# Kernel tuning notes

Measured on AMD Instinct MI355X. Metric: run time of the kernel, lower is better.

Reference implementation:

```python
import jax, jax.numpy as jnp
import numpy as np

B = 2_000_000   # time steps (the module's 'batch' axis is the sequential time axis)
SEQ = 1
IN = 2
SPIN = 365
TRAIN = 1_000_000


def setup_inputs() -> dict:
    key = jax.random.key(0)
    ks = jax.random.split(key, 9)
    x = jax.random.uniform(ks[0], (B, SEQ, IN), dtype=jnp.float32)
    y_obs = jax.random.uniform(ks[1], (B, 1), dtype=jnp.float32)
    c_mean = jax.random.uniform(ks[2], (1,), dtype=jnp.float32)
    c_std = jax.random.uniform(ks[3], (1,), dtype=jnp.float32) + 0.5  # keep away from 0
    weight_r_yom = jax.random.uniform(ks[4], (1, 1), dtype=jnp.float32)
    weight_r_ylm = jax.random.uniform(ks[5], (1, 1), dtype=jnp.float32)
    weight_r_yfm = jax.random.uniform(ks[6], (1, 1), dtype=jnp.float32)
    bias_b0_yom = jax.random.uniform(ks[7], (1,), dtype=jnp.float32)
    weight_b1_yom = jax.random.uniform(ks[8], (1, 1), dtype=jnp.float32)
    return dict(x=x, epoch=1, time_lag=0, y_obs=y_obs, c_mean=c_mean, c_std=c_std,
                weight_r_yom=weight_r_yom, weight_r_ylm=weight_r_ylm,
                weight_r_yfm=weight_r_yfm, bias_b0_yom=bias_b0_yom,
                weight_b1_yom=weight_b1_yom)


def _forward(x, y_obs, c_mean, c_std, weight_r_yom, weight_r_ylm, weight_r_yfm,
             bias_b0_yom, weight_b1_yom, time_lag):
    # hidden_size == 1 -> scalar cell state. Original loop order: b outer, t inner,
    # i.e. steps visit x[b, t] in row-major order; per-b outputs keep the last t value.
    Bn, S, _ = x.shape
    steps = x.reshape(Bn * S, 2)[time_lag * S:]            # rows b < time_lag are skipped
    wo, wl, wf = weight_r_yom[0, 0], weight_r_ylm[0, 0], weight_r_yfm[0, 0]
    b0, wb1 = bias_b0_yom[0], weight_b1_yom[0, 0]
    mo, so = c_mean[0], c_std[0]
    eo, el, ef = jnp.exp(wo), jnp.exp(wl), jnp.exp(wf)
    denom = eo + el + ef
    oo1 = eo / denom                                        # softmax-like gate weights
    ol1 = el / denom
    obsstd = jnp.std(y_obs[SPIN:TRAIN], ddof=1)             # torch.std is unbiased (ddof=1)

    def step(c, u):
        u1, u2 = u[0], u[1]
        oo = oo1 * jax.nn.sigmoid(b0 + (c - mo) / so * wb1)  # output gate
        safe_c = jnp.where(c > 0, c, jnp.float32(1.0))
        olc = jnp.where(c > 0, ol1 - jax.nn.relu(ol1 - u2 / safe_c), ol1)  # PET-clamped leak
        f = 1.0 - oo - olc                                   # mass-conserving forget gate
        c_next = f * c + u1
        # per-step stored values use the PRE-update state c (c_0 in original)
        return c_next, (oo * c, c, ol1 * c, olc * c, oo, olc, f)

    _, (q, cs, ls, lcs, goo, golc, gf) = jax.lax.scan(step, jnp.float32(0.0), steps)

    def per_b(v):
        v = v.reshape(-1, S)[:, -1]          # keep last inner-t value per b
        v = jnp.pad(v, (time_lag, 0))        # skipped rows stay zero
        return v[:, None]                    # [B, 1]

    h_n = per_b(q)                           # bp_0 == 0, so h_n == q_n == oo * c_0
    c_n = per_b(cs)
    l_n = per_b(ls)
    lc_n = per_b(lcs)
    Gate_oo = per_b(goo)
    Gate_olc = per_b(golc)
    Gate_f = per_b(gf)
    processed = (jnp.arange(Bn)[:, None] >= time_lag)
    Gate_ol = jnp.where(processed, ol1, 0.0).astype(x.dtype)
    obs_std = jnp.where(processed, obsstd, 0.0).astype(x.dtype)
    zeros = jnp.zeros((Bn, 1), x.dtype)      # bp_n and Gate_ib (ib == 0 always)
    h_nout = jnp.concatenate([h_n, obs_std], axis=1)
    return (h_n, c_n, l_n, lc_n, zeros, zeros, Gate_oo, Gate_ol, Gate_olc, Gate_f,
            h_nout, obs_std)


def reference(x, epoch, time_lag, y_obs, c_mean, c_std, weight_r_yom, weight_r_ylm,
              weight_r_yfm, bias_b0_yom, weight_b1_yom):
    return _forward(x, y_obs, c_mean, c_std, weight_r_yom, weight_r_ylm,
                    weight_r_yfm, bias_b0_yom, weight_b1_yom, int(time_lag))
```

## Files before the change

### kernel.cpp

```cpp
#include <hip/hip_runtime.h>
#include <math.h>

#define SPIN 365
#define TRAIN 1000000
#define WARM 64
#define L 8
#define BLK 512
#define RPB (L * BLK)
#define NSTAGE (RPB + WARM)
#define NPART 256


__global__ void partial_std_kernel(const float* __restrict__ y, double* __restrict__ part) {
    int tid = blockIdx.x * blockDim.x + threadIdx.x;
    int stride = gridDim.x * blockDim.x;
    double s = 0.0, s2 = 0.0;
    for (int i = SPIN + tid; i < TRAIN; i += stride) {
        double v = (double)y[i];
        s += v;
        s2 += v * v;
    }
    for (int off = 32; off > 0; off >>= 1) {
        s  += __shfl_down(s,  off, 64);
        s2 += __shfl_down(s2, off, 64);
    }
    __shared__ double ls[4], ls2[4];
    int lane = threadIdx.x & 63, w = threadIdx.x >> 6;
    if (lane == 0) { ls[w] = s; ls2[w] = s2; }
    __syncthreads();
    if (threadIdx.x == 0) {
        double ts = 0.0, ts2 = 0.0;
        int nw = blockDim.x >> 6;
        for (int i = 0; i < nw; ++i) { ts += ls[i]; ts2 += ls2[i]; }
        part[2 * blockIdx.x]     = ts;
        part[2 * blockIdx.x + 1] = ts2;
    }
}


struct Par { float oo1, ol1, ez1, ez0; };

__device__ __forceinline__ void step_state(float& c, float u1, float u2, const Par p) {
    float e   = __builtin_amdgcn_exp2f(fmaf(c, p.ez1, p.ez0));
    float sg  = __builtin_amdgcn_rcpf(1.0f + e);
    float ooc = p.oo1 * sg * c;
    float lc  = p.ol1 * c;
    float mlc = (c > 0.0f) ? fminf(lc, u2) : lc;
    c = c - ooc - mlc + u1;
}

__device__ __forceinline__ void gates(float c, float u2, const Par p,
                                      float& oo, float& olc, float& f) {
    float e  = __builtin_amdgcn_exp2f(fmaf(c, p.ez1, p.ez0));
    float sg = __builtin_amdgcn_rcpf(1.0f + e);
    oo = p.oo1 * sg;
    float rc = __builtin_amdgcn_rcpf(c);
    float q  = u2 * rc;
    float olc_pos = fminf(p.ol1, q);
    olc = (c > 0.0f) ? olc_pos : p.ol1;
    f = 1.0f - oo - olc;
}

__device__ __forceinline__ void ldu(const float* __restrict__ up, int off,
                                    float& a, float& b) {
    int idx = 2 * off + (off >> 4);
    a = up[idx];
    b = up[idx + 1];
}

__global__ __launch_bounds__(BLK, 4)
void scan_kernel(const float* __restrict__ x,
                 const int*  __restrict__ time_lag_p,
                 const float* __restrict__ cm, const float* __restrict__ cs,
                 const float* __restrict__ wro, const float* __restrict__ wrl,
                 const float* __restrict__ wrf, const float* __restrict__ b0p,
                 const float* __restrict__ wb1p,
                 const double* __restrict__ part,
                 float* __restrict__ out, int Btot) {
    __shared__ float s_x[2 * NSTAGE + NSTAGE / 16];
    __shared__ float s_cpre[BLK * (L + 1)];
    __shared__ float s_ostd;

    const long long Bl = (long long)Btot;
    const int tl  = time_lag_p[0];
    const int tid = threadIdx.x;

    {
        long long gstride = (long long)gridDim.x * BLK;
        for (long long b = (long long)blockIdx.x * BLK + tid; b < tl; b += gstride) {
            for (int s = 0; s < 10; ++s) out[(long long)s * Bl + b] = 0.0f;
            out[10 * Bl + 2 * b]     = 0.0f;
            out[10 * Bl + 2 * b + 1] = 0.0f;
            out[12 * Bl + b] = 0.0f;
        }
    }

    const float wo = wro[0], wl = wrl[0], wf = wrf[0];
    const float b0 = b0p[0], wb1 = wb1p[0], mo = cm[0], so = cs[0];
    const float eo = __expf(wo), el = __expf(wl), ef = __expf(wf);
    const float denom = eo + el + ef;
    const float kz1 = wb1 / so;
    const float kz0 = b0 - mo * kz1;
    const float LOG2E = 1.4426950408889634f;
    Par par;
    par.oo1 = eo / denom;
    par.ol1 = el / denom;
    par.ez1 = -kz1 * LOG2E;
    par.ez0 = -kz0 * LOG2E;
    const float ol1 = par.ol1;

    const long long row0    = (long long)tl + (long long)blockIdx.x * RPB;
    const long long base    = row0 - WARM;
    const long long lastrow = Bl - 1;

    #pragma unroll
    for (int k = 0; k < (NSTAGE + BLK - 1) / BLK; ++k) {
        int off = k * BLK + tid;
        if (off < NSTAGE) {
            long long row = base + off;
            row = row < 0 ? 0 : (row > lastrow ? lastrow : row);
            float2 v = *(const float2*)(x + 2 * row);
            int idx = 2 * off + (off >> 4);
            s_x[idx]     = v.x;
            s_x[idx + 1] = v.y;
        }
    }
    __syncthreads();

    if (tid < 64) {
        double s = 0.0, s2 = 0.0;
        for (int i = tid; i < NPART; i += 64) {
            s  += part[2 * i];
            s2 += part[2 * i + 1];
        }
        for (int off = 32; off > 0; off >>= 1) {
            s  += __shfl_down(s,  off, 64);
            s2 += __shfl_down(s2, off, 64);
        }
        if (tid == 0) {
            double n = (double)(TRAIN - SPIN);
            double var = (s2 - s * s / n) / (n - 1.0);
            s_ostd = (float)sqrt(var);
        }
    }

    {
        const long long r0 = row0 + (long long)tid * L;
        if (r0 < Bl) {
            long long wstart = r0 - WARM;
            if (wstart < tl) wstart = tl;
            const int nwarm = (int)(r0 - wstart);
            long long lenl = Bl - r0;
            const int len = lenl > L ? L : (int)lenl;
            const int off0 = (int)(wstart - base);

            float c = 0.0f;
            float aA[8], bA[8], aB[8], bB[8];

            if (nwarm == WARM) {
                #pragma unroll
                for (int q = 0; q < 8; ++q) ldu(s_x, off0 + q, aA[q], bA[q]);
                #pragma unroll
                for (int g = 0; g < 4; ++g) {
                    #pragma unroll
                    for (int q = 0; q < 8; ++q) ldu(s_x, off0 + (2 * g + 1) * 8 + q, aB[q], bB[q]);
                    #pragma unroll
                    for (int q = 0; q < 8; ++q) step_state(c, aA[q], bA[q], par);
                    #pragma unroll
                    for (int q = 0; q < 8; ++q) ldu(s_x, off0 + (2 * g + 2) * 8 + q, aA[q], bA[q]);
                    #pragma unroll
                    for (int q = 0; q < 8; ++q) step_state(c, aB[q], bB[q], par);
                }
            } else {
                for (int s = 0; s < nwarm; ++s) {
                    float ua, ub;
                    ldu(s_x, off0 + s, ua, ub);
                    step_state(c, ua, ub, par);
                }
                #pragma unroll
                for (int q = 0; q < 8; ++q) ldu(s_x, off0 + nwarm + q, aA[q], bA[q]);
            }

            float* myld = s_cpre + tid * (L + 1);
            #pragma unroll
            for (int j = 0; j < L; ++j) {
                if (j < len) myld[j] = c;
                step_state(c, aA[j], bA[j], par);
            }
        }
    }

    __syncthreads();

    const float ostd = s_ostd;
    const bool aligned = ((tl & 3) == 0);
    const float4 z4  = make_float4(0.0f, 0.0f, 0.0f, 0.0f);
    const float4 ol4 = make_float4(ol1, ol1, ol1, ol1);
    const float4 os4 = make_float4(ostd, ostd, ostd, ostd);

    #pragma unroll
    for (int p = 0; p < L / 4; ++p) {
        const int rl = p * (BLK * 4) + tid * 4;
        const long long r = row0 + rl;
        if (r >= Bl) continue;

        float cp[4], u2v[4];
        #pragma unroll
        for (int e = 0; e < 4; ++e) {
            int rle = rl + e;
            cp[e] = s_cpre[(rle >> 3) * (L + 1) + (rle & 7)];
            float ua, ub;
            ldu(s_x, rl + e + WARM, ua, ub);
            u2v[e] = ub;
        }

        if (aligned && (r + 3 < Bl)) {
            float h[4], lo[4], lc[4], go[4], gc[4], gf[4];
            #pragma unroll
            for (int e = 0; e < 4; ++e) {
                float oo, olc, f;
                gates(cp[e], u2v[e], par, oo, olc, f);
                h[e]  = oo * cp[e];
                lo[e] = ol1 * cp[e];
                lc[e] = olc * cp[e];
                go[e] = oo;
                gc[e] = olc;
                gf[e] = f;
            }
            *(float4*)(out + r)          = make_float4(h[0], h[1], h[2], h[3]);
            *(float4*)(out + Bl + r)     = make_float4(cp[0], cp[1], cp[2], cp[3]);
            *(float4*)(out + 2 * Bl + r) = make_float4(lo[0], lo[1], lo[2], lo[3]);
            *(float4*)(out + 3 * Bl + r) = make_float4(lc[0], lc[1], lc[2], lc[3]);
            *(float4*)(out + 4 * Bl + r) = z4;
            *(float4*)(out + 5 * Bl + r) = z4;
            *(float4*)(out + 6 * Bl + r) = make_float4(go[0], go[1], go[2], go[3]);
            *(float4*)(out + 7 * Bl + r) = ol4;
            *(float4*)(out + 8 * Bl + r) = make_float4(gc[0], gc[1], gc[2], gc[3]);
            *(float4*)(out + 9 * Bl + r) = make_float4(gf[0], gf[1], gf[2], gf[3]);
            *(float4*)(out + 10 * Bl + 2 * r)     = make_float4(h[0], ostd, h[1], ostd);
            *(float4*)(out + 10 * Bl + 2 * r + 4) = make_float4(h[2], ostd, h[3], ostd);
            *(float4*)(out + 12 * Bl + r) = os4;
        } else {
            #pragma unroll
            for (int e = 0; e < 4; ++e) {
                long long t = r + e;
                if (t >= Bl) break;
                float oo, olc, f;
                gates(cp[e], u2v[e], par, oo, olc, f);
                float h = oo * cp[e];
                out[t]           = h;
                out[Bl + t]      = cp[e];
                out[2 * Bl + t]  = ol1 * cp[e];
                out[3 * Bl + t]  = olc * cp[e];
                out[4 * Bl + t]  = 0.0f;
                out[5 * Bl + t]  = 0.0f;
                out[6 * Bl + t]  = oo;
                out[7 * Bl + t]  = ol1;
                out[8 * Bl + t]  = olc;
                out[9 * Bl + t]  = f;
                out[10 * Bl + 2 * t]     = h;
                out[10 * Bl + 2 * t + 1] = ostd;
                out[12 * Bl + t] = ostd;
            }
        }
    }
}


extern "C" void kernel_launch(void* const* d_in, const int* in_sizes, int n_in,
                              void* d_out, int out_size, void* d_ws, size_t ws_size,
                              hipStream_t stream) {
    const float* x        = (const float*)d_in[0];
    const int*   time_lag = (const int*)d_in[2];
    const float* y_obs    = (const float*)d_in[3];
    const float* c_mean   = (const float*)d_in[4];
    const float* c_std    = (const float*)d_in[5];
    const float* w_yom    = (const float*)d_in[6];
    const float* w_ylm    = (const float*)d_in[7];
    const float* w_yfm    = (const float*)d_in[8];
    const float* b0       = (const float*)d_in[9];
    const float* wb1      = (const float*)d_in[10];
    float* out = (float*)d_out;

    const int B = in_sizes[0] / 2;

    double* part = (double*)d_ws;

    partial_std_kernel<<<NPART, 256, 0, stream>>>(y_obs, part);

    const int blocks = (B + RPB - 1) / RPB;
    scan_kernel<<<blocks, BLK, 0, stream>>>(x, time_lag, c_mean, c_std,
                                            w_yom, w_ylm, w_yfm, b0, wb1,
                                            part, out, B);
}
```

Baseline: 154.4 us.

## Make each wavefront process an independent tile to drop block-wide barriers

Restructures the scan kernel so each 64-lane wavefront owns its own 512-row tile with private shared-memory staging for inputs and per-thread starting states. Both __syncthreads calls go away, and every wavefront computes the obs_std reduction redundantly instead of sharing it through shared memory. The time_lag zero-fill is skipped when time_lag is zero. The aim is to let wavefronts run out of lock-step and hide load latency. The cost is more warm-up overhead per tile, since tiles are smaller, and duplicated reads of the partial sums.

```diff
diff --git a/kernel.cpp b/kernel.cpp
--- a/kernel.cpp
+++ b/kernel.cpp
@@ -4,10 +4,12 @@
 #define SPIN 365
 #define TRAIN 1000000
 #define WARM 64
-#define L 8
+#define TPW 512
 #define BLK 512
-#define RPB (L * BLK)
-#define NSTAGE (RPB + WARM)
+#define WPB (BLK / 64)
+#define XROWS (TPW + WARM)
+#define XSEG (2 * XROWS + XROWS / 16)
+#define CSEG (64 * 9)
 #define NPART 256
 
 
@@ -77,15 +79,16 @@
                  const float* __restrict__ wb1p,
                  const double* __restrict__ part,
                  float* __restrict__ out, int Btot) {
-    __shared__ float s_x[2 * NSTAGE + NSTAGE / 16];
-    __shared__ float s_cpre[BLK * (L + 1)];
-    __shared__ float s_ostd;
+    __shared__ float s_x[WPB * XSEG];
+    __shared__ float s_c[WPB * CSEG];
 
     const long long Bl = (long long)Btot;
-    const int tl  = time_lag_p[0];
-    const int tid = threadIdx.x;
-
-    {
+    const int tl   = time_lag_p[0];
+    const int tid  = threadIdx.x;
+    const int wid  = tid >> 6;
+    const int lane = tid & 63;
+
+    if (tl > 0) {
         long long gstride = (long long)gridDim.x * BLK;
         for (long long b = (long long)blockIdx.x * BLK + tid; b < tl; b += gstride) {
             for (int s = 0; s < 10; ++s) out[(long long)s * Bl + b] = 0.0f;
@@ -94,6 +97,10 @@
             out[12 * Bl + b] = 0.0f;
         }
     }
+
+    const long long gw = (long long)blockIdx.x * WPB + wid;
+    const long long r0 = (long long)tl + gw * TPW;
+    if (r0 >= Bl) return;
 
     const float wo = wro[0], wl = wrl[0], wf = wrf[0];
     const float b0 = b0p[0], wb1 = wb1p[0], mo = cm[0], so = cs[0];
@@ -109,49 +116,44 @@
     par.ez0 = -kz0 * LOG2E;
     const float ol1 = par.ol1;
 
-    const long long row0    = (long long)tl + (long long)blockIdx.x * RPB;
-    const long long base    = row0 - WARM;
+    double s = 0.0, s2 = 0.0;
+    for (int i = lane; i < NPART; i += 64) {
+        s  += part[2 * i];
+        s2 += part[2 * i + 1];
+    }
+    for (int off = 32; off > 0; off >>= 1) {
+        s  += __shfl_down(s,  off, 64);
+        s2 += __shfl_down(s2, off, 64);
+    }
+    s  = __shfl(s, 0, 64);
+    s2 = __shfl(s2, 0, 64);
+    const double nn = (double)(TRAIN - SPIN);
+    const float ostd = (float)sqrt((s2 - s * s / nn) / (nn - 1.0));
+
+    const long long base    = r0 - WARM;
     const long long lastrow = Bl - 1;
+    float* sx = s_x + wid * XSEG;
+    float* sc = s_c + wid * CSEG;
 
     #pragma unroll
-    for (int k = 0; k < (NSTAGE + BLK - 1) / BLK; ++k) {
-        int off = k * BLK + tid;
-        if (off < NSTAGE) {
-            long long row = base + off;
-            row = row < 0 ? 0 : (row > lastrow ? lastrow : row);
-            float2 v = *(const float2*)(x + 2 * row);
-            int idx = 2 * off + (off >> 4);
-            s_x[idx]     = v.x;
-            s_x[idx + 1] = v.y;
-        }
-    }
-    __syncthreads();
-
-    if (tid < 64) {
-        double s = 0.0, s2 = 0.0;
-        for (int i = tid; i < NPART; i += 64) {
-            s  += part[2 * i];
-            s2 += part[2 * i + 1];
-        }
-        for (int off = 32; off > 0; off >>= 1) {
-            s  += __shfl_down(s,  off, 64);
-            s2 += __shfl_down(s2, off, 64);
-        }
-        if (tid == 0) {
-            double n = (double)(TRAIN - SPIN);
-            double var = (s2 - s * s / n) / (n - 1.0);
-            s_ostd = (float)sqrt(var);
-        }
+    for (int k = 0; k < XROWS / 64; ++k) {
+        int off = k * 64 + lane;
+        long long row = base + off;
+        row = row < 0 ? 0 : (row > lastrow ? lastrow : row);
+        float2 v = *(const float2*)(x + 2 * row);
+        int idx = 2 * off + (off >> 4);
+        sx[idx]     = v.x;
+        sx[idx + 1] = v.y;
     }
 
     {
-        const long long r0 = row0 + (long long)tid * L;
-        if (r0 < Bl) {
-            long long wstart = r0 - WARM;
+        const long long rt = r0 + (long long)lane * 8;
+        if (rt < Bl) {
+            long long wstart = rt - WARM;
             if (wstart < tl) wstart = tl;
-            const int nwarm = (int)(r0 - wstart);
-            long long lenl = Bl - r0;
-            const int len = lenl > L ? L : (int)lenl;
+            const int nwarm = (int)(rt - wstart);
+            long long lenl = Bl - rt;
+            const int len = lenl > 8 ? 8 : (int)lenl;
             const int off0 = (int)(wstart - base);
 
             float c = 0.0f;
@@ -159,75 +161,73 @@
 
             if (nwarm == WARM) {
                 #pragma unroll
-                for (int q = 0; q < 8; ++q) ldu(s_x, off0 + q, aA[q], bA[q]);
+                for (int q = 0; q < 8; ++q) ldu(sx, off0 + q, aA[q], bA[q]);
                 #pragma unroll
                 for (int g = 0; g < 4; ++g) {
                     #pragma unroll
-                    for (int q = 0; q < 8; ++q) ldu(s_x, off0 + (2 * g + 1) * 8 + q, aB[q], bB[q]);
+                    for (int q = 0; q < 8; ++q) ldu(sx, off0 + (2 * g + 1) * 8 + q, aB[q], bB[q]);
                     #pragma unroll
                     for (int q = 0; q < 8; ++q) step_state(c, aA[q], bA[q], par);
                     #pragma unroll
-                    for (int q = 0; q < 8; ++q) ldu(s_x, off0 + (2 * g + 2) * 8 + q, aA[q], bA[q]);
+                    for (int q = 0; q < 8; ++q) ldu(sx, off0 + (2 * g + 2) * 8 + q, aA[q], bA[q]);
                     #pragma unroll
                     for (int q = 0; q < 8; ++q) step_state(c, aB[q], bB[q], par);
                 }
             } else {
-                for (int s = 0; s < nwarm; ++s) {
+                for (int t = 0; t < nwarm; ++t) {
                     float ua, ub;
-                    ldu(s_x, off0 + s, ua, ub);
+                    ldu(sx, off0 + t, ua, ub);
                     step_state(c, ua, ub, par);
                 }
                 #pragma unroll
-                for (int q = 0; q < 8; ++q) ldu(s_x, off0 + nwarm + q, aA[q], bA[q]);
-            }
-
-            float* myld = s_cpre + tid * (L + 1);
+                for (int q = 0; q < 8; ++q) ldu(sx, off0 + nwarm + q, aA[q], bA[q]);
+            }
+
+            float* my = sc + lane * 9;
             #pragma unroll
-            for (int j = 0; j < L; ++j) {
-                if (j < len) myld[j] = c;
+            for (int j = 0; j < 8; ++j) {
+                if (j < len) my[j] = c;
                 step_state(c, aA[j], bA[j], par);
             }
         }
     }
 
-    __syncthreads();
-
-    const float ostd = s_ostd;
     const bool aligned = ((tl & 3) == 0);
     const float4 z4  = make_float4(0.0f, 0.0f, 0.0f, 0.0f);
     const float4 ol4 = make_float4(ol1, ol1, ol1, ol1);
     const float4 os4 = make_float4(ostd, ostd, ostd, ostd);
 
     #pragma unroll
-    for (int p = 0; p < L / 4; ++p) {
-        const int rl = p * (BLK * 4) + tid * 4;
-        const long long r = row0 + rl;
+    for (int h = 0; h < 2; ++h) {
+        const int rl = h * 256 + lane * 4;
+        const long long r = r0 + rl;
         if (r >= Bl) continue;
 
+        const int sidx = rl >> 3;
+        const int j0   = (lane & 1) * 4;
         float cp[4], u2v[4];
         #pragma unroll
         for (int e = 0; e < 4; ++e) {
-            int rle = rl + e;
-            cp[e] = s_cpre[(rle >> 3) * (L + 1) + (rle & 7)];
+            cp[e] = sc[sidx * 9 + j0 + e];
             float ua, ub;
-            ldu(s_x, rl + e + WARM, ua, ub);
+            ldu(sx, WARM + rl + e, ua, ub);
             u2v[e] = ub;
         }
 
         if (aligned && (r + 3 < Bl)) {
-            float h[4], lo[4], lc[4], go[4], gc[4], gf[4];
+            float h4[4], lo[4], lc[4], go[4], gc[4], gf[4];
             #pragma unroll
             for (int e = 0; e < 4; ++e) {
                 float oo, olc, f;
                 gates(cp[e], u2v[e], par, oo, olc, f);
-                h[e]  = oo * cp[e];
+                h4[e] = oo * cp[e];
                 lo[e] = ol1 * cp[e];
                 lc[e] = olc * cp[e];
                 go[e] = oo;
                 gc[e] = olc;
                 gf[e] = f;
             }
-            *(float4*)(out + r)          = make_float4(h[0], h[1], h[2], h[3]);
+            *(float4*)(out + r)          = make_float4(h4[0], h4[1], h4[2], h4[3]);
             *(float4*)(out + Bl + r)     = make_float4(cp[0], cp[1], cp[2], cp[3]);
             *(float4*)(out + 2 * Bl + r) = make_float4(lo[0], lo[1], lo[2], lo[3]);
             *(float4*)(out + 3 * Bl + r) = make_float4(lc[0], lc[1], lc[2], lc[3]);
@@ -237,8 +237,8 @@
             *(float4*)(out + 7 * Bl + r) = ol4;
             *(float4*)(out + 8 * Bl + r) = make_float4(gc[0], gc[1], gc[2], gc[3]);
             *(float4*)(out + 9 * Bl + r) = make_float4(gf[0], gf[1], gf[2], gf[3]);
-            *(float4*)(out + 10 * Bl + 2 * r)     = make_float4(h[0], ostd, h[1], ostd);
-            *(float4*)(out + 10 * Bl + 2 * r + 4) = make_float4(h[2], ostd, h[3], ostd);
+            *(float4*)(out + 10 * Bl + 2 * r)     = make_float4(h4[0], ostd, h4[1], ostd);
+            *(float4*)(out + 10 * Bl + 2 * r + 4) = make_float4(h4[2], ostd, h4[3], ostd);
             *(float4*)(out + 12 * Bl + r) = os4;
         } else {
             #pragma unroll
@@ -247,8 +247,8 @@
                 if (t >= Bl) break;
                 float oo, olc, f;
                 gates(cp[e], u2v[e], par, oo, olc, f);
-                float h = oo * cp[e];
-                out[t]           = h;
+                float hh = oo * cp[e];
+                out[t]           = hh;
                 out[Bl + t]      = cp[e];
                 out[2 * Bl + t]  = ol1 * cp[e];
                 out[3 * Bl + t]  = olc * cp[e];
@@ -258,7 +258,7 @@
                 out[7 * Bl + t]  = ol1;
                 out[8 * Bl + t]  = olc;
                 out[9 * Bl + t]  = f;
-                out[10 * Bl + 2 * t]     = h;
+                out[10 * Bl + 2 * t]     = hh;
                 out[10 * Bl + 2 * t + 1] = ostd;
                 out[12 * Bl + t] = ostd;
             }
@@ -288,7 +288,8 @@
 
     partial_std_kernel<<<NPART, 256, 0, stream>>>(y_obs, part);
 
-    const int blocks = (B + RPB - 1) / RPB;
+    const long long ntiles = ((long long)B + TPW - 1) / TPW;
+    const int blocks = (int)((ntiles + WPB - 1) / WPB);
     scan_kernel<<<blocks, BLK, 0, stream>>>(x, time_lag, c_mean, c_std,
                                             w_yom, w_ylm, w_yfm, b0, wb1,
                                             part, out, B);
```

Measured after the change: 151.1 us, median of 2. -2.1%, faster.
